# Optimization experiments

Hardware: AMD Instinct MI355X
Metric: run time of the kernel (lower is better)

Reference implementation:

```python
import jax, jax.numpy as jnp
import numpy as np

N_SEG = 128      # number of ragged segments (len(leng))
TOTAL = 32768    # total rows = sum(leng)
D = 1280         # cnn_feature (tf_efficientnet_b0 classifier.in_features)
D_HEAD = 512     # hidden of logits head


def setup_inputs() -> dict:
    key = jax.random.key(0)
    ks = jax.random.split(key, 8)
    # ragged lengths (static at trace time), summing exactly to TOTAL
    rng = np.random.default_rng(0)
    leng = rng.integers(64, 448, size=N_SEG).astype(np.int64)
    leng = np.maximum((leng * (TOTAL / leng.sum())).astype(np.int64), 1)
    leng[-1] += TOTAL - leng.sum()
    segment_ids = jnp.asarray(np.repeat(np.arange(N_SEG), leng), jnp.int32)

    features = jax.random.normal(ks[0], (TOTAL, D), jnp.float32)
    s = 0.02
    Ww = jax.random.normal(ks[1], (D, D), jnp.float32) * s        # proj_w.weight
    bw = jnp.zeros((D,), jnp.float32)                              # proj_w.bias
    v = jax.random.normal(ks[2], (D,), jnp.float32) * s           # proj_v.weight (1,D) squeezed
    W1 = jax.random.normal(ks[3], (D_HEAD, D), jnp.float32) * s   # logits[0].weight
    b1 = jnp.zeros((D_HEAD,), jnp.float32)
    W2 = jax.random.normal(ks[4], (1, D_HEAD), jnp.float32) * s   # logits[3].weight
    b2 = jnp.zeros((1,), jnp.float32)
    return {"features": features, "Ww": Ww, "bw": bw, "v": v,
            "W1": W1, "b1": b1, "W2": W2, "b2": b2,
            "segment_ids": segment_ids}


def reference(features, Ww, bw, v, W1, b1, W2, b2, segment_ids):
    # per-row attention logits: tanh(x @ Ww^T + bw) @ v    -> [TOTAL]
    H = jnp.tanh(features @ Ww.T + bw)
    s = H @ v
    # segment-wise stable softmax (replaces Python loop over leng)
    m = jax.ops.segment_max(s, segment_ids, num_segments=N_SEG)
    e = jnp.exp(s - m[segment_ids])
    z = jax.ops.segment_sum(e, segment_ids, num_segments=N_SEG)
    att = e / z[segment_ids]                                      # [TOTAL]
    # attention-weighted sum pooling per segment -> [N_SEG, D]
    pooled = jax.ops.segment_sum(features * att[:, None], segment_ids,
                                 num_segments=N_SEG)
    # logits head (dropout is identity in eval)
    h = jax.nn.relu(pooled @ W1.T + b1)
    return h @ W2.T + b2                                          # [N_SEG, 1]
```

## Files before the change

kernel.cpp:

```cpp
#include <hip/hip_runtime.h>
#include <hip/hip_bf16.h>


#define TOTAL_ROWS 32768
#define DIM 1280
#define NSEG 128
#define DHEAD 512

typedef _Float16 f16x8 __attribute__((ext_vector_type(8)));
typedef float f32x4 __attribute__((ext_vector_type(4)));

#define OFF_XH   0
#define OFF_WH   83886080
#define OFF_S    87162880
#define OFF_ATT  87293952
#define OFF_SEG  87425024
#define OFF_POOL 87426048
#define OFF_H    88081408

__device__ __forceinline__ void load_lds16(const void* g, void* l) {
  __builtin_amdgcn_global_load_lds(
      (const __attribute__((address_space(1))) unsigned int*)g,
      (__attribute__((address_space(3))) unsigned int*)l, 16, 0, 0);
}

__device__ __forceinline__ float tanh_fast(float x) {
  float e = __expf(2.0f * x);
  return 1.0f - 2.0f * __builtin_amdgcn_rcpf(e + 1.0f);
}

__global__ void cvt_f16_kernel(const float* __restrict__ in,
                               _Float16* __restrict__ out, int n8) {
  int i = blockIdx.x * blockDim.x + threadIdx.x;
  if (i >= n8) return;
  const float4* p = (const float4*)in + (size_t)i * 2;
  float4 u0 = p[0], u1 = p[1];
  f16x8 h;
  h[0] = (_Float16)u0.x; h[1] = (_Float16)u0.y;
  h[2] = (_Float16)u0.z; h[3] = (_Float16)u0.w;
  h[4] = (_Float16)u1.x; h[5] = (_Float16)u1.y;
  h[6] = (_Float16)u1.z; h[7] = (_Float16)u1.w;
  *((f16x8*)out + i) = h;
}

__global__ void segstart_kernel(const int* __restrict__ sid,
                                int* __restrict__ segstart, int total) {
  int i = blockIdx.x * blockDim.x + threadIdx.x;
  if (i >= total) return;
  int sg = sid[i];
  if (i == 0) segstart[0] = 0;
  else if (sid[i - 1] != sg) segstart[sg] = i;
  if (i == total - 1) segstart[sg + 1] = total;
}

__global__ __launch_bounds__(256) void gemm_s_kernel(
    const _Float16* __restrict__ X, const _Float16* __restrict__ W,
    const float* __restrict__ v, const float* __restrict__ bw,
    float* __restrict__ s) {
  __shared__ _Float16 As[128 * 32];
  __shared__ _Float16 Bs[128 * 32];
  const int rowBase = blockIdx.x * 128;
  const int jBase = blockIdx.y * 128;
  const int t = threadIdx.x;
  const int lane = t & 63;
  const int w = t >> 6;
  const int wm = w & 1, wn = w >> 1;

  f32x4 acc[4][4];
  const f32x4 zero = {0.f, 0.f, 0.f, 0.f};
#pragma unroll
  for (int i = 0; i < 4; ++i)
#pragma unroll
    for (int j = 0; j < 4; ++j) acc[i][j] = zero;

  for (int k0 = 0; k0 < DIM; k0 += 32) {
    __syncthreads();
#pragma unroll
    for (int q = 0; q < 2; ++q) {
      int c = w * 128 + q * 64 + lane;
      int row = c >> 2, c16 = c & 3;
      load_lds16(X + (size_t)(rowBase + row) * DIM + k0 + c16 * 8,
                 &As[(size_t)(w * 128 + q * 64) * 8]);
      load_lds16(W + (size_t)(jBase + row) * DIM + k0 + c16 * 8,
                 &Bs[(size_t)(w * 128 + q * 64) * 8]);
    }
    __syncthreads();

    f16x8 a[4], b[4];
    const int kb = (lane >> 4) * 8;
#pragma unroll
    for (int mt = 0; mt < 4; ++mt)
      a[mt] = *(const f16x8*)&As[(wm * 64 + mt * 16 + (lane & 15)) * 32 + kb];
#pragma unroll
    for (int nt = 0; nt < 4; ++nt)
      b[nt] = *(const f16x8*)&Bs[(wn * 64 + nt * 16 + (lane & 15)) * 32 + kb];
#pragma unroll
    for (int mt = 0; mt < 4; ++mt)
#pragma unroll
      for (int nt = 0; nt < 4; ++nt)
        acc[mt][nt] =
            __builtin_amdgcn_mfma_f32_16x16x32_f16(a[mt], b[nt], acc[mt][nt], 0, 0, 0);
  }

  const int colBase = jBase + wn * 64 + (lane & 15);
  float vv[4], bb[4];
#pragma unroll
  for (int nt = 0; nt < 4; ++nt) {
    int j = colBase + nt * 16;
    vv[nt] = v[j];
    bb[nt] = bw[j];
  }
  const int g = lane >> 4;
#pragma unroll
  for (int mt = 0; mt < 4; ++mt) {
#pragma unroll
    for (int r = 0; r < 4; ++r) {
      float sumv = 0.f;
#pragma unroll
      for (int nt = 0; nt < 4; ++nt)
        sumv += tanh_fast(acc[mt][nt][r] + bb[nt]) * vv[nt];
      sumv += __shfl_xor(sumv, 1);
      sumv += __shfl_xor(sumv, 2);
      sumv += __shfl_xor(sumv, 4);
      sumv += __shfl_xor(sumv, 8);
      if ((lane & 15) == 0) {
        int row = rowBase + wm * 64 + mt * 16 + g * 4 + r;
        atomicAdd(&s[row], sumv);
      }
    }
  }
}

__global__ void softmax_kernel(const float* __restrict__ s,
                               const int* __restrict__ segstart,
                               float* __restrict__ att) {
  int seg = blockIdx.x;
  int st = segstart[seg], en = segstart[seg + 1];
  int t = threadIdx.x;
  __shared__ float red[8];
  float m = -1e30f;
  for (int i = st + t; i < en; i += 256) m = fmaxf(m, s[i]);
  for (int d = 1; d < 64; d <<= 1) m = fmaxf(m, __shfl_xor(m, d));
  if ((t & 63) == 0) red[t >> 6] = m;
  __syncthreads();
  m = fmaxf(fmaxf(red[0], red[1]), fmaxf(red[2], red[3]));
  float z = 0.f;
  for (int i = st + t; i < en; i += 256) z += __expf(s[i] - m);
  for (int d = 1; d < 64; d <<= 1) z += __shfl_xor(z, d);
  if ((t & 63) == 0) red[4 + (t >> 6)] = z;
  __syncthreads();
  z = red[4] + red[5] + red[6] + red[7];
  float rz = 1.0f / z;
  for (int i = st + t; i < en; i += 256) att[i] = __expf(s[i] - m) * rz;
}

__global__ void pool_kernel(const float* __restrict__ F,
                            const float* __restrict__ att,
                            const int* __restrict__ segstart,
                            float* __restrict__ pooled) {
  int seg = blockIdx.y;
  int col = blockIdx.x * 256 + threadIdx.x;
  int st = segstart[seg], en = segstart[seg + 1];
  float acc = 0.f;
  int r = st;
  for (; r + 4 <= en; r += 4) {
    acc = fmaf(att[r], F[(size_t)r * DIM + col], acc);
    acc = fmaf(att[r + 1], F[(size_t)(r + 1) * DIM + col], acc);
    acc = fmaf(att[r + 2], F[(size_t)(r + 2) * DIM + col], acc);
    acc = fmaf(att[r + 3], F[(size_t)(r + 3) * DIM + col], acc);
  }
  for (; r < en; ++r) acc = fmaf(att[r], F[(size_t)r * DIM + col], acc);
  pooled[(size_t)seg * DIM + col] = acc;
}

__global__ void head1_kernel(const float* __restrict__ pooled,
                             const float* __restrict__ W1,
                             const float* __restrict__ b1, float* __restrict__ h) {
  int og = blockIdx.x, sg = blockIdx.y;
  __shared__ float Wt[16 * 65];
  __shared__ float Pt[32 * 65];
  int t = threadIdx.x;
  int tx = t & 15, ty = t >> 4;
  float acc0 = 0.f, acc1 = 0.f;
  for (int kc = 0; kc < 20; ++kc) {
    __syncthreads();
#pragma unroll
    for (int u = 0; u < 4; ++u) {
      int lin = t + 256 * u;
      int o = lin >> 6, kk = lin & 63;
      Wt[o * 65 + kk] = W1[(size_t)(og * 16 + o) * DIM + kc * 64 + kk];
    }
#pragma unroll
    for (int u = 0; u < 8; ++u) {
      int lin = t + 256 * u;
      int ss = lin >> 6, kk = lin & 63;
      Pt[ss * 65 + kk] = pooled[(size_t)(sg * 32 + ss) * DIM + kc * 64 + kk];
    }
    __syncthreads();
#pragma unroll
    for (int kk = 0; kk < 64; ++kk) {
      float wv = Wt[tx * 65 + kk];
      acc0 = fmaf(Pt[ty * 65 + kk], wv, acc0);
      acc1 = fmaf(Pt[(ty + 16) * 65 + kk], wv, acc1);
    }
  }
  int o = og * 16 + tx;
  float bias = b1[o];
  h[(size_t)(sg * 32 + ty) * DHEAD + o] = fmaxf(acc0 + bias, 0.f);
  h[(size_t)(sg * 32 + ty + 16) * DHEAD + o] = fmaxf(acc1 + bias, 0.f);
}

__global__ void head2_kernel(const float* __restrict__ h,
                             const float* __restrict__ W2,
                             const float* __restrict__ b2, float* __restrict__ out) {
  int seg = blockIdx.x;
  int t = threadIdx.x;
  float val = h[(size_t)seg * DHEAD + t] * W2[t] +
              h[(size_t)seg * DHEAD + t + 256] * W2[t + 256];
  for (int d = 1; d < 64; d <<= 1) val += __shfl_xor(val, d);
  __shared__ float red[4];
  if ((t & 63) == 0) red[t >> 6] = val;
  __syncthreads();
  if (t == 0) out[seg] = red[0] + red[1] + red[2] + red[3] + b2[0];
}

extern "C" void kernel_launch(void* const* d_in, const int* in_sizes, int n_in,
                              void* d_out, int out_size, void* d_ws, size_t ws_size,
                              hipStream_t stream) {
  const float* features = (const float*)d_in[0];
  const float* Ww = (const float*)d_in[1];
  const float* bw = (const float*)d_in[2];
  const float* v = (const float*)d_in[3];
  const float* W1 = (const float*)d_in[4];
  const float* b1 = (const float*)d_in[5];
  const float* W2 = (const float*)d_in[6];
  const float* b2 = (const float*)d_in[7];
  const int* segids = (const int*)d_in[8];
  float* out = (float*)d_out;

  char* ws = (char*)d_ws;
  _Float16* Xh = (_Float16*)(ws + OFF_XH);
  _Float16* Wh = (_Float16*)(ws + OFF_WH);
  float* s = (float*)(ws + OFF_S);
  float* att = (float*)(ws + OFF_ATT);
  int* segstart = (int*)(ws + OFF_SEG);
  float* pooled = (float*)(ws + OFF_POOL);
  float* h = (float*)(ws + OFF_H);

  hipMemsetAsync(s, 0, TOTAL_ROWS * sizeof(float), stream);

  cvt_f16_kernel<<<20480, 256, 0, stream>>>(features, Xh, TOTAL_ROWS * DIM / 8);
  cvt_f16_kernel<<<800, 256, 0, stream>>>(Ww, Wh, DIM * DIM / 8);
  segstart_kernel<<<TOTAL_ROWS / 256, 256, 0, stream>>>(segids, segstart, TOTAL_ROWS);

  dim3 ggrid(TOTAL_ROWS / 128, DIM / 128);
  gemm_s_kernel<<<ggrid, 256, 0, stream>>>(Xh, Wh, v, bw, s);

  softmax_kernel<<<NSEG, 256, 0, stream>>>(s, segstart, att);
  pool_kernel<<<dim3(DIM / 256, NSEG), 256, 0, stream>>>(features, att, segstart, pooled);
  head1_kernel<<<dim3(32, 4), 256, 0, stream>>>(pooled, W1, b1, h);
  head2_kernel<<<NSEG, 256, 0, stream>>>(h, W2, b2, out);
}
```

Baseline: 520.6 us.

## Double GEMM K-tile with swizzled LDS layout and split pooling rows with atomics

The score GEMM now stages 64-wide K slices per iteration, halving the number of barrier pairs. It uses an XOR-like rotation of 16-byte chunks in LDS to avoid bank conflicts on the MFMA operand reads. The pooling kernel is restructured so each block covers a quarter of a segment's rows across all 1280 columns with float4 loads, then accumulates into a zeroed pooled buffer with atomics. This trades more LDS per block and atomic traffic for fewer syncs and wider memory accesses.

```diff
diff --git a/kernel.cpp b/kernel.cpp
--- a/kernel.cpp
+++ b/kernel.cpp
@@ -57,8 +57,8 @@
     const _Float16* __restrict__ X, const _Float16* __restrict__ W,
     const float* __restrict__ v, const float* __restrict__ bw,
     float* __restrict__ s) {
-  __shared__ _Float16 As[128 * 32];
-  __shared__ _Float16 Bs[128 * 32];
+  __shared__ _Float16 As[128 * 64];
+  __shared__ _Float16 Bs[128 * 64];
   const int rowBase = blockIdx.x * 128;
   const int jBase = blockIdx.y * 128;
   const int t = threadIdx.x;
@@ -73,33 +73,44 @@
 #pragma unroll
     for (int j = 0; j < 4; ++j) acc[i][j] = zero;
 
-  for (int k0 = 0; k0 < DIM; k0 += 32) {
-    __syncthreads();
-#pragma unroll
-    for (int q = 0; q < 2; ++q) {
-      int c = w * 128 + q * 64 + lane;
-      int row = c >> 2, c16 = c & 3;
-      load_lds16(X + (size_t)(rowBase + row) * DIM + k0 + c16 * 8,
-                 &As[(size_t)(w * 128 + q * 64) * 8]);
-      load_lds16(W + (size_t)(jBase + row) * DIM + k0 + c16 * 8,
-                 &Bs[(size_t)(w * 128 + q * 64) * 8]);
-    }
-    __syncthreads();
-
-    f16x8 a[4], b[4];
-    const int kb = (lane >> 4) * 8;
-#pragma unroll
-    for (int mt = 0; mt < 4; ++mt)
-      a[mt] = *(const f16x8*)&As[(wm * 64 + mt * 16 + (lane & 15)) * 32 + kb];
-#pragma unroll
-    for (int nt = 0; nt < 4; ++nt)
-      b[nt] = *(const f16x8*)&Bs[(wn * 64 + nt * 16 + (lane & 15)) * 32 + kb];
-#pragma unroll
-    for (int mt = 0; mt < 4; ++mt)
-#pragma unroll
-      for (int nt = 0; nt < 4; ++nt)
-        acc[mt][nt] =
-            __builtin_amdgcn_mfma_f32_16x16x32_f16(a[mt], b[nt], acc[mt][nt], 0, 0, 0);
+  for (int k0 = 0; k0 < DIM; k0 += 64) {
+    __syncthreads();
+#pragma unroll
+    for (int q = 0; q < 4; ++q) {
+      int l = w * 256 + q * 64 + lane;
+      int row = l >> 3;
+      int g = ((l & 7) - row) & 7;
+      load_lds16(X + (size_t)(rowBase + row) * DIM + k0 + g * 8,
+                 &As[(size_t)(w * 256 + q * 64) * 8]);
+      load_lds16(W + (size_t)(jBase + row) * DIM + k0 + g * 8,
+                 &Bs[(size_t)(w * 256 + q * 64) * 8]);
+    }
+    __syncthreads();
+
+    f16x8 a[2][4], b[2][4];
+    const int kc = lane >> 4;
+#pragma unroll
+    for (int s2 = 0; s2 < 2; ++s2) {
+      int q = s2 * 4 + kc;
+#pragma unroll
+      for (int mt = 0; mt < 4; ++mt) {
+        int row = wm * 64 + mt * 16 + (lane & 15);
+        a[s2][mt] = *(const f16x8*)&As[row * 64 + ((q + row) & 7) * 8];
+      }
+#pragma unroll
+      for (int nt = 0; nt < 4; ++nt) {
+        int row = wn * 64 + nt * 16 + (lane & 15);
+        b[s2][nt] = *(const f16x8*)&Bs[row * 64 + ((q + row) & 7) * 8];
+      }
+    }
+#pragma unroll
+    for (int s2 = 0; s2 < 2; ++s2)
+#pragma unroll
+      for (int mt = 0; mt < 4; ++mt)
+#pragma unroll
+        for (int nt = 0; nt < 4; ++nt)
+          acc[mt][nt] = __builtin_amdgcn_mfma_f32_16x16x32_f16(
+              a[s2][mt], b[s2][nt], acc[mt][nt], 0, 0, 0);
   }
 
   const int colBase = jBase + wn * 64 + (lane & 15);
@@ -158,19 +169,34 @@
                             const float* __restrict__ att,
                             const int* __restrict__ segstart,
                             float* __restrict__ pooled) {
-  int seg = blockIdx.y;
-  int col = blockIdx.x * 256 + threadIdx.x;
+  int seg = blockIdx.x, part = blockIdx.y;
   int st = segstart[seg], en = segstart[seg + 1];
-  float acc = 0.f;
-  int r = st;
-  for (; r + 4 <= en; r += 4) {
-    acc = fmaf(att[r], F[(size_t)r * DIM + col], acc);
-    acc = fmaf(att[r + 1], F[(size_t)(r + 1) * DIM + col], acc);
-    acc = fmaf(att[r + 2], F[(size_t)(r + 2) * DIM + col], acc);
-    acc = fmaf(att[r + 3], F[(size_t)(r + 3) * DIM + col], acc);
-  }
-  for (; r < en; ++r) acc = fmaf(att[r], F[(size_t)r * DIM + col], acc);
-  pooled[(size_t)seg * DIM + col] = acc;
+  int len = en - st;
+  int chunk = (len + 3) >> 2;
+  int r0 = st + chunk * part;
+  int r1 = min(en, r0 + chunk);
+  int t = threadIdx.x;
+  f32x4 acc = {0.f, 0.f, 0.f, 0.f};
+  int r = r0;
+  for (; r + 2 <= r1; r += 2) {
+    float a0 = att[r], a1 = att[r + 1];
+    f32x4 f0 = ((const f32x4*)(F + (size_t)r * DIM))[t];
+    f32x4 f1 = ((const f32x4*)(F + (size_t)(r + 1) * DIM))[t];
+#pragma unroll
+    for (int c = 0; c < 4; ++c) {
+      acc[c] = fmaf(a0, f0[c], acc[c]);
+      acc[c] = fmaf(a1, f1[c], acc[c]);
+    }
+  }
+  if (r < r1) {
+    float a0 = att[r];
+    f32x4 f0 = ((const f32x4*)(F + (size_t)r * DIM))[t];
+#pragma unroll
+    for (int c = 0; c < 4; ++c) acc[c] = fmaf(a0, f0[c], acc[c]);
+  }
+  float* dst = pooled + (size_t)seg * DIM + t * 4;
+#pragma unroll
+  for (int c = 0; c < 4; ++c) atomicAdd(dst + c, acc[c]);
 }
 
 __global__ void head1_kernel(const float* __restrict__ pooled,
@@ -248,6 +274,7 @@
   float* h = (float*)(ws + OFF_H);
 
   hipMemsetAsync(s, 0, TOTAL_ROWS * sizeof(float), stream);
+  hipMemsetAsync(pooled, 0, NSEG * DIM * sizeof(float), stream);
 
   cvt_f16_kernel<<<20480, 256, 0, stream>>>(features, Xh, TOTAL_ROWS * DIM / 8);
   cvt_f16_kernel<<<800, 256, 0, stream>>>(Ww, Wh, DIM * DIM / 8);
@@ -257,7 +284,7 @@
   gemm_s_kernel<<<ggrid, 256, 0, stream>>>(Xh, Wh, v, bw, s);
 
   softmax_kernel<<<NSEG, 256, 0, stream>>>(s, segstart, att);
-  pool_kernel<<<dim3(DIM / 256, NSEG), 256, 0, stream>>>(features, att, segstart, pooled);
+  pool_kernel<<<dim3(NSEG, 4), 320, 0, stream>>>(features, att, segstart, pooled);
   head1_kernel<<<dim3(32, 4), 256, 0, stream>>>(pooled, W1, b1, h);
   head2_kernel<<<NSEG, 256, 0, stream>>>(h, W2, b2, out);
 }
```

After: 480.0 us. -7.8%, faster.
